# Kernel optimization log

Measured on AMD Instinct MI355X. Metric: run time of the kernel, lower is better.

## Reference

```python
import jax, jax.numpy as jnp
import numpy as np

S_CENTROIDS = 512
RADIUS = 0.5
NSAMPLE = 32
BN_EPS = 1e-5


def farthest_point_sample(xyz, s):
    # xyz: [B, N, 3] -> idx [B, s], deterministic start at index 0
    B, N, _ = xyz.shape

    def step(carry, _):
        dist, far = carry  # dist [B,N], far [B]
        centroid = jnp.take_along_axis(xyz, far[:, None, None], axis=1)  # [B,1,3]
        d = jnp.sum((xyz - centroid) ** 2, axis=-1)  # [B,N]
        dist = jnp.minimum(dist, d)
        nxt = jnp.argmax(dist, axis=-1).astype(jnp.int32)
        return (dist, nxt), far

    init = (jnp.full((B, N), 1e10, dtype=xyz.dtype), jnp.zeros((B,), jnp.int32))
    _, idx = jax.lax.scan(step, init, None, length=s)
    return idx.T  # [B, s]


def query_ball_point(radius, nsample, xyz, new_xyz):
    # xyz [B,N,3], new_xyz [B,S,3] -> group idx [B,S,nsample]
    B, N, _ = xyz.shape
    sqr = jnp.sum((new_xyz[:, :, None, :] - xyz[:, None, :, :]) ** 2, axis=-1)  # [B,S,N]
    gidx = jnp.where(sqr > radius * radius, N, jnp.arange(N, dtype=jnp.int32)[None, None, :])
    gidx = jnp.sort(gidx, axis=-1)[:, :, :nsample]  # closest-index-first valid ids
    first = gidx[:, :, :1]
    gidx = jnp.where(gidx == N, first, gidx)  # pad misses with first neighbor
    return gidx


def bn_relu(h, gamma, beta):
    # training-mode BatchNorm1d over (batch, length) dims of [BS, C, k]
    m = jnp.mean(h, axis=(0, 2), keepdims=True)
    v = jnp.var(h, axis=(0, 2), keepdims=True)
    hn = (h - m) / jnp.sqrt(v + BN_EPS)
    return jax.nn.relu(hn * gamma[None, :, None] + beta[None, :, None])


def setup_inputs() -> dict:
    key = jax.random.key(0)
    k1, k2, k3, k4 = jax.random.split(key, 4)
    B, N, Din, Dout = 16, 2048, 64, 128  # in_channels=2*Din=128
    x = jax.random.normal(k1, (B, Din, N), dtype=jnp.float32)
    coords = jax.random.uniform(k2, (B, N, 3), dtype=jnp.float32, minval=-1.0, maxval=1.0)
    W1 = jax.random.normal(k3, (Dout, 2 * Din), dtype=jnp.float32) * 0.05  # conv1 1x1 kernel
    W2 = jax.random.normal(k4, (Dout, Dout), dtype=jnp.float32) * 0.05    # conv2 1x1 kernel
    gamma1 = jnp.ones((Dout,), jnp.float32); beta1 = jnp.zeros((Dout,), jnp.float32)
    gamma2 = jnp.ones((Dout,), jnp.float32); beta2 = jnp.zeros((Dout,), jnp.float32)
    return {"x": x, "coords": coords, "W1": W1, "W2": W2,
            "gamma1": gamma1, "beta1": beta1, "gamma2": gamma2, "beta2": beta2}


def reference(x, coords, W1, W2, gamma1, beta1, gamma2, beta2):
    B = x.shape[0]
    feats = jnp.transpose(x, (0, 2, 1))  # [B, N, D]

    fidx = farthest_point_sample(coords, S_CENTROIDS)  # [B, s]
    bidx = jnp.arange(B)[:, None]
    new_xyz = coords[bidx, fidx]        # [B, s, 3]
    new_feat = feats[bidx, fidx]        # [B, s, D]

    gidx = query_ball_point(RADIUS, NSAMPLE, coords, new_xyz)  # [B, s, k]
    grouped = feats[jnp.arange(B)[:, None, None], gidx]        # [B, s, k, D]

    center = new_feat[:, :, None, :]
    agg = jnp.concatenate([grouped - center,
                           jnp.broadcast_to(center, grouped.shape)], axis=-1)  # [B, s, k, 2D]

    b, s, k, d = agg.shape
    h = jnp.transpose(agg, (0, 1, 3, 2)).reshape(b * s, d, k)  # [BS, 2D, k]
    h = bn_relu(jnp.einsum('bck,oc->bok', h, W1), gamma1, beta1)
    h = bn_relu(jnp.einsum('bck,oc->bok', h, W2), gamma2, beta2)
    pooled = jnp.max(h, axis=-1)                  # [BS, out]
    new_feature = jnp.transpose(pooled.reshape(b, s, -1), (0, 2, 1))  # [B, out, s]
    return new_xyz, new_feature
```

## Files before the change

### kernel.cpp

```cpp
#include <hip/hip_runtime.h>
#include <cstdint>

typedef unsigned int uint;
typedef unsigned short ushort_t;
typedef unsigned long long ull;
typedef __attribute__((ext_vector_type(8))) short bf16x8;
typedef __attribute__((ext_vector_type(4))) float f32x4;

#define B_   16
#define N_   2048
#define S_   512
#define G_   8192
#define DIN  64
#define DOUT 128
#define K_   32
#define ATS  136
#define ATS1 72

__device__ __forceinline__ uint bf16b(float f) {
  uint u = __float_as_uint(f);
  return (u + 0x7fffu + ((u >> 16) & 1u)) >> 16;
}
__device__ __forceinline__ float bf2f(uint b) { return __uint_as_float(b << 16); }

template<int CTRL, int RM>
__device__ __forceinline__ ull dpp_max_step(ull x) {
  uint lo = (uint)x, hi = (uint)(x >> 32);
  uint nlo = (uint)__builtin_amdgcn_update_dpp((int)lo, (int)lo, CTRL, RM, 0xf, true);
  uint nhi = (uint)__builtin_amdgcn_update_dpp((int)hi, (int)hi, CTRL, RM, 0xf, true);
  ull y = ((ull)nhi << 32) | (ull)nlo;
  return x > y ? x : y;
}

__global__ __launch_bounds__(256) void fps_kernel(const float* __restrict__ coords,
                                                  int* __restrict__ fidx,
                                                  float* __restrict__ out_xyz) {
  int b = blockIdx.x;
  const float* cb = coords + (size_t)b * (N_ * 3);
  __shared__ float4 spt[N_];
  __shared__ ull    skey[2][4];
  __shared__ int    sfar[S_];
  int tid = threadIdx.x, wid = tid >> 6;
  float px[8], py[8], pz[8], dist[8];
  uint nidx[8];
  int j0 = tid * 8;
#pragma unroll
  for (int i = 0; i < 8; ++i) {
    float x3 = cb[3 * (j0 + i)], y3 = cb[3 * (j0 + i) + 1], z3 = cb[3 * (j0 + i) + 2];
    px[i] = x3; py[i] = y3; pz[i] = z3;
    spt[j0 + i] = make_float4(x3, y3, z3, 0.f);
    dist[i] = 1e10f;
    nidx[i] = ~(uint)(j0 + i);
  }
  float cx = cb[0], cy = cb[1], cz = cb[2];
  uint far = 0;
  __syncthreads();
  for (int s = 0; s < S_; ++s) {
    if (tid == 0) sfar[s] = (int)far;
    ull best = 0;
#pragma unroll
    for (int i = 0; i < 8; ++i) {
      float dx = __fsub_rn(px[i], cx);
      float dy = __fsub_rn(py[i], cy);
      float dz = __fsub_rn(pz[i], cz);
      float d = __fadd_rn(__fadd_rn(__fmul_rn(dx, dx), __fmul_rn(dy, dy)), __fmul_rn(dz, dz));
      float nd = fminf(dist[i], d);
      dist[i] = nd;
      ull p = ((ull)__float_as_uint(nd) << 32) | (ull)nidx[i];
      best = best > p ? best : p;
    }
    best = dpp_max_step<0x111, 0xf>(best);
    best = dpp_max_step<0x112, 0xf>(best);
    best = dpp_max_step<0x114, 0xf>(best);
    best = dpp_max_step<0x118, 0xf>(best);
    best = dpp_max_step<0x142, 0xa>(best);
    best = dpp_max_step<0x143, 0xc>(best);
    int pb = s & 1;
    if ((tid & 63) == 63) skey[pb][wid] = best;
    __syncthreads();
    ull k0 = skey[pb][0], k1 = skey[pb][1], k2 = skey[pb][2], k3 = skey[pb][3];
    uint jw0 = ~(uint)k0, jw1 = ~(uint)k1, jw2 = ~(uint)k2, jw3 = ~(uint)k3;
    float4 q0 = spt[jw0], q1 = spt[jw1], q2 = spt[jw2], q3 = spt[jw3];
    bool t01 = k0 > k1, t23 = k2 > k3;
    ull ka = t01 ? k0 : k1;   float4 qa = t01 ? q0 : q1;
    ull kb2 = t23 ? k2 : k3;  float4 qb = t23 ? q2 : q3;
    bool tw = ka > kb2;
    ull kw = tw ? ka : kb2;   float4 qw = tw ? qa : qb;
    far = ~(uint)kw;
    cx = qw.x; cy = qw.y; cz = qw.z;
  }
  __syncthreads();
  for (int s2 = tid; s2 < S_; s2 += 256) {
    int f = sfar[s2];
    fidx[b * S_ + s2] = f;
    float4 c4 = spt[f];
    int o = (b * S_ + s2) * 3;
    out_xyz[o] = c4.x; out_xyz[o + 1] = c4.y; out_xyz[o + 2] = c4.z;
  }
}

__global__ __launch_bounds__(256) void ball_kernel(const float* __restrict__ coords,
                                                   const int* __restrict__ fidx,
                                                   int* __restrict__ gidx) {
  int lane = threadIdx.x & 63;
  int g = __builtin_amdgcn_readfirstlane(blockIdx.x * 4 + (threadIdx.x >> 6));
  int b = g >> 9;
  const float* cb = coords + (size_t)b * (N_ * 3);
  int nf = fidx[g];
  float cx = cb[3 * nf], cy = cb[3 * nf + 1], cz = cb[3 * nf + 2];
  int* out = gidx + g * K_;
  int cnt = 0, first = 0;
  bool hasfirst = false;
  for (int base = 0; base < N_; base += 64) {
    int j = base + lane;
    float dx = __fsub_rn(cb[3 * j], cx);
    float dy = __fsub_rn(cb[3 * j + 1], cy);
    float dz = __fsub_rn(cb[3 * j + 2], cz);
    float d = __fadd_rn(__fadd_rn(__fmul_rn(dx, dx), __fmul_rn(dy, dy)), __fmul_rn(dz, dz));
    bool in = (d <= 0.25f);
    ull m = __ballot(in);
    if (in) {
      int pos = cnt + __popcll(m & ((1ull << lane) - 1ull));
      if (pos < K_) out[pos] = j;
    }
    if (!hasfirst && m) { first = base + (__ffsll((long long)m) - 1); hasfirst = true; }
    cnt += __popcll(m);
    if (cnt >= K_) break;
  }
  if (cnt < K_) {
    for (int p = cnt + lane; p < K_; p += 64) out[p] = first;
  }
}

__global__ __launch_bounds__(256) void prep_kernel(const float* __restrict__ W1,
                                                   const float* __restrict__ W2,
                                                   ushort_t* __restrict__ Bp1,
                                                   ushort_t* __restrict__ Bpd,
                                                   ushort_t* __restrict__ Bp2) {
  int i = blockIdx.x * 256 + threadIdx.x;
  int j2 = i & 7, l = (i >> 3) & 63;
  {
    int kc = (i >> 9) & 3, nt = i >> 11;
    int o2 = nt * 16 + (l & 15);
    int c2 = kc * 32 + ((l >> 4) * 8) + j2;
    Bp2[i] = (ushort_t)bf16b(W2[o2 * 128 + c2]);
  }
  if (i < 8192) {
    int kc = (i >> 9) & 1, nt = (i >> 10) & 7;
    int o2 = nt * 16 + (l & 15);
    int c2 = kc * 32 + ((l >> 4) * 8) + j2;
    float wa = W1[o2 * 128 + c2];
    float wb = W1[o2 * 128 + 64 + c2];
    Bp1[i] = (ushort_t)bf16b(wa);
    Bpd[i] = (ushort_t)bf16b(wb - wa);
  }
}

__global__ __launch_bounds__(256) void gemm1_kernel(const float* __restrict__ x,
    const int* __restrict__ fidx, const int* __restrict__ gidx,
    const ushort_t* __restrict__ Bp1, const ushort_t* __restrict__ Bpd,
    ushort_t* __restrict__ h1T, float* __restrict__ psum, float* __restrict__ psq) {
  __shared__ ushort_t xgT[4][32 * ATS1];
  __shared__ float sctr[4][DIN];
  int tid = threadIdx.x;
  int lane = tid & 63, wid = tid >> 6;
  int g = __builtin_amdgcn_readfirstlane(blockIdx.x * 4 + wid);
  int b = g >> 9;
  const float* xb = x + (size_t)b * (DIN * N_);
  int nf = fidx[g];
  sctr[wid][lane] = xb[(size_t)lane * N_ + nf];
  int kk = lane & 31, ch = lane >> 5;
  int gik = gidx[g * K_ + kk];
  ushort_t* xw = xgT[wid];
#pragma unroll
  for (int cc = 0; cc < 32; ++cc) {
    int c = ch * 32 + cc;
    xw[kk * ATS1 + c] = (ushort_t)bf16b(xb[(size_t)c * N_ + gik]);
  }
  __syncthreads();
  int l15 = lane & 15, r8 = (lane >> 4) * 8;
  f32x4 acc[2][8];
#pragma unroll
  for (int nt = 0; nt < 8; ++nt) acc[0][nt] = (f32x4){0.f, 0.f, 0.f, 0.f};
#pragma unroll
  for (int kc = 0; kc < 2; ++kc) {
    union { bf16x8 v; ushort_t u[8]; } cu;
#pragma unroll
    for (int j = 0; j < 8; ++j) cu.u[j] = (ushort_t)bf16b(sctr[wid][kc * 32 + r8 + j]);
#pragma unroll
    for (int nt = 0; nt < 8; ++nt) {
      bf16x8 bf = *(const bf16x8*)(Bpd + ((nt * 2 + kc) * 64 + lane) * 8);
      acc[0][nt] = __builtin_amdgcn_mfma_f32_16x16x32_bf16(cu.v, bf, acc[0][nt], 0, 0, 0);
    }
  }
#pragma unroll
  for (int nt = 0; nt < 8; ++nt) acc[1][nt] = acc[0][nt];
#pragma unroll
  for (int kc = 0; kc < 2; ++kc) {
    bf16x8 afrag[2];
#pragma unroll
    for (int mt = 0; mt < 2; ++mt)
      afrag[mt] = *(const bf16x8*)(xw + (mt * 16 + l15) * ATS1 + kc * 32 + r8);
#pragma unroll
    for (int nt = 0; nt < 8; ++nt) {
      bf16x8 bf = *(const bf16x8*)(Bp1 + ((nt * 2 + kc) * 64 + lane) * 8);
      acc[0][nt] = __builtin_amdgcn_mfma_f32_16x16x32_bf16(afrag[0], bf, acc[0][nt], 0, 0, 0);
      acc[1][nt] = __builtin_amdgcn_mfma_f32_16x16x32_bf16(afrag[1], bf, acc[1][nt], 0, 0, 0);
    }
  }
#pragma unroll
  for (int nt = 0; nt < 8; ++nt) {
    float s = 0.f, q = 0.f;
#pragma unroll
    for (int mt = 0; mt < 2; ++mt)
#pragma unroll
      for (int r = 0; r < 4; ++r) { float a = acc[mt][nt][r]; s += a; q = fmaf(a, a, q); }
    s += __shfl_xor(s, 16, 64); s += __shfl_xor(s, 32, 64);
    q += __shfl_xor(q, 16, 64); q += __shfl_xor(q, 32, 64);
    if (lane < 16) {
      int o = nt * 16 + lane;
      psum[o * G_ + g] = s; psq[o * G_ + g] = q;
    }
  }
#pragma unroll
  for (int mt = 0; mt < 2; ++mt)
#pragma unroll
    for (int r = 0; r < 4; ++r) {
      int k = mt * 16 + (lane >> 4) * 4 + r;
      ushort_t* dst = h1T + (size_t)g * 4096 + k * 128 + l15;
#pragma unroll
      for (int nt = 0; nt < 8; ++nt)
        dst[nt * 16] = (ushort_t)bf16b(acc[mt][nt][r]);
    }
}

__global__ __launch_bounds__(256) void bn_finalize(const float* __restrict__ psum,
    const float* __restrict__ psq, const float* __restrict__ gamma,
    const float* __restrict__ beta, float* __restrict__ bnp) {
  int o = blockIdx.x, tid = threadIdx.x;
  double s = 0.0, q = 0.0;
  for (int g = tid; g < G_; g += 256) { s += (double)psum[o * G_ + g]; q += (double)psq[o * G_ + g]; }
  __shared__ double ss[256], qq[256];
  ss[tid] = s; qq[tid] = q; __syncthreads();
  for (int off = 128; off > 0; off >>= 1) {
    if (tid < off) { ss[tid] += ss[tid + off]; qq[tid] += qq[tid + off]; }
    __syncthreads();
  }
  if (tid == 0) {
    double n = 262144.0;
    double mean = ss[0] / n, var = qq[0] / n - mean * mean;
    float scv = (float)((double)gamma[o] / sqrt(var + 1e-5));
    bnp[2 * o] = scv;
    bnp[2 * o + 1] = (float)((double)beta[o] - mean * (double)scv);
  }
}

__global__ __launch_bounds__(256) void gemm2_kernel(const ushort_t* __restrict__ h1T,
    const ushort_t* __restrict__ Bp2, const float* __restrict__ bnp1,
    float* __restrict__ psum, float* __restrict__ psq,
    float* __restrict__ hmax, float* __restrict__ hmin) {
  __shared__ ushort_t actT[4][32 * ATS];
  int tid = threadIdx.x;
  int lane = tid & 63, wid = tid >> 6;
  int g = __builtin_amdgcn_readfirstlane(blockIdx.x * 4 + wid);
  ushort_t* aw = actT[wid];
  int c0 = (lane & 15) * 8;
  float s1[8], t1[8];
#pragma unroll
  for (int jj = 0; jj < 8; ++jj) { s1[jj] = bnp1[2 * (c0 + jj)]; t1[jj] = bnp1[2 * (c0 + jj) + 1]; }
  const uint4* src = (const uint4*)(h1T + (size_t)g * 4096);
#pragma unroll
  for (int t = 0; t < 8; ++t) {
    int idx = t * 64 + lane;
    uint4 v = src[idx];
    int k = idx >> 4;
    uint w[4] = {v.x, v.y, v.z, v.w};
    uint o4[4];
#pragma unroll
    for (int p2 = 0; p2 < 4; ++p2) {
      float a0 = fmaxf(fmaf(bf2f(w[p2] & 0xffffu), s1[2 * p2], t1[2 * p2]), 0.f);
      float a1 = fmaxf(fmaf(bf2f(w[p2] >> 16), s1[2 * p2 + 1], t1[2 * p2 + 1]), 0.f);
      o4[p2] = (bf16b(a1) << 16) | bf16b(a0);
    }
    *(uint4*)(aw + k * ATS + c0) = make_uint4(o4[0], o4[1], o4[2], o4[3]);
  }
  __syncthreads();
  f32x4 acc[2][8];
#pragma unroll
  for (int mt = 0; mt < 2; ++mt)
#pragma unroll
    for (int nt = 0; nt < 8; ++nt) acc[mt][nt] = (f32x4){0.f, 0.f, 0.f, 0.f};
#pragma unroll
  for (int kc = 0; kc < 4; ++kc) {
    bf16x8 afrag[2];
#pragma unroll
    for (int mt = 0; mt < 2; ++mt)
      afrag[mt] = *(const bf16x8*)(aw + (mt * 16 + (lane & 15)) * ATS + kc * 32 + (lane >> 4) * 8);
#pragma unroll
    for (int nt = 0; nt < 8; ++nt) {
      bf16x8 bfrag = *(const bf16x8*)(Bp2 + ((nt * 4 + kc) * 64 + lane) * 8);
      acc[0][nt] = __builtin_amdgcn_mfma_f32_16x16x32_bf16(afrag[0], bfrag, acc[0][nt], 0, 0, 0);
      acc[1][nt] = __builtin_amdgcn_mfma_f32_16x16x32_bf16(afrag[1], bfrag, acc[1][nt], 0, 0, 0);
    }
  }
#pragma unroll
  for (int nt = 0; nt < 8; ++nt) {
    float s = 0.f, q = 0.f, mx = -1e30f, mn = 1e30f;
#pragma unroll
    for (int mt = 0; mt < 2; ++mt)
#pragma unroll
      for (int r = 0; r < 4; ++r) {
        float a = acc[mt][nt][r];
        s += a; q = fmaf(a, a, q); mx = fmaxf(mx, a); mn = fminf(mn, a);
      }
    s += __shfl_xor(s, 16, 64); s += __shfl_xor(s, 32, 64);
    q += __shfl_xor(q, 16, 64); q += __shfl_xor(q, 32, 64);
    mx = fmaxf(mx, __shfl_xor(mx, 16, 64)); mx = fmaxf(mx, __shfl_xor(mx, 32, 64));
    mn = fminf(mn, __shfl_xor(mn, 16, 64)); mn = fminf(mn, __shfl_xor(mn, 32, 64));
    if (lane < 16) {
      int o = nt * 16 + lane;
      psum[o * G_ + g] = s; psq[o * G_ + g] = q;
      hmax[o * G_ + g] = mx; hmin[o * G_ + g] = mn;
    }
  }
}

__global__ __launch_bounds__(256) void pool_kernel(const float* __restrict__ hmax,
    const float* __restrict__ hmin, const float* __restrict__ bnp2,
    float* __restrict__ out) {
  int i = blockIdx.x * 256 + threadIdx.x;
  int s = i & 511;
  int o = (i >> 9) & 127;
  int b = i >> 16;
  int g = b * 512 + s;
  float scv = bnp2[2 * o], tf = bnp2[2 * o + 1];
  float v = (scv >= 0.f) ? hmax[o * G_ + g] : hmin[o * G_ + g];
  out[i] = fmaxf(fmaf(scv, v, tf), 0.f);
}

extern "C" void kernel_launch(void* const* d_in, const int* in_sizes, int n_in,
                              void* d_out, int out_size, void* d_ws, size_t ws_size,
                              hipStream_t stream) {
  const float* x      = (const float*)d_in[0];
  const float* coords = (const float*)d_in[1];
  const float* W1     = (const float*)d_in[2];
  const float* W2     = (const float*)d_in[3];
  const float* gamma1 = (const float*)d_in[4];
  const float* beta1  = (const float*)d_in[5];
  const float* gamma2 = (const float*)d_in[6];
  const float* beta2  = (const float*)d_in[7];
  float* out = (float*)d_out;
  char* ws = (char*)d_ws;
  ushort_t* h1T  = (ushort_t*)(ws);
  float* psum1 = (float*)(ws + 67108864);
  float* psq1  = (float*)(ws + 71303168);
  float* psum2 = (float*)(ws + 75497472);
  float* psq2  = (float*)(ws + 79691776);
  float* hmax  = (float*)(ws + 83886080);
  float* hmin  = (float*)(ws + 88080384);
  ushort_t* Bp1 = (ushort_t*)(ws + 92274688);
  ushort_t* Bpd = (ushort_t*)(ws + 92291072);
  ushort_t* Bp2 = (ushort_t*)(ws + 92307456);
  float* bnp1  = (float*)(ws + 92340224);
  float* bnp2  = (float*)(ws + 92341248);
  int* fidx    = (int*)(ws + 92342272);
  int* gidx    = (int*)(ws + 92375040);

  prep_kernel<<<64, 256, 0, stream>>>(W1, W2, Bp1, Bpd, Bp2);
  fps_kernel<<<16, 256, 0, stream>>>(coords, fidx, out);
  ball_kernel<<<2048, 256, 0, stream>>>(coords, fidx, gidx);
  gemm1_kernel<<<2048, 256, 0, stream>>>(x, fidx, gidx, Bp1, Bpd, h1T, psum1, psq1);
  bn_finalize<<<128, 256, 0, stream>>>(psum1, psq1, gamma1, beta1, bnp1);
  gemm2_kernel<<<2048, 256, 0, stream>>>(h1T, Bp2, bnp1, psum2, psq2, hmax, hmin);
  bn_finalize<<<128, 256, 0, stream>>>(psum2, psq2, gamma2, beta2, bnp2);
  pool_kernel<<<4096, 256, 0, stream>>>(hmax, hmin, bnp2, out + 24576);
}
```

Before: 387.2 us.

## Use packed f32 math and float-only wave argmax in FPS kernel

Rewrites the farthest-point-sampling inner loop to compute squared distances with packed v_pk_add/mul_f32 on pairs of points. It replaces the 64-bit key DPP max reduction with a 32-bit float max, followed by a ballot and readlane to recover the winning lane and local index. Point coordinates in shared memory move from float4 AoS to SoA. The goal is to shorten the serial per-iteration critical path, at the cost of extra readlane/ballot steps and subtler tie-breaking, since the lowest lane wins ties.

```diff
diff --git a/kernel.cpp b/kernel.cpp
--- a/kernel.cpp
+++ b/kernel.cpp
@@ -6,6 +6,7 @@
 typedef unsigned long long ull;
 typedef __attribute__((ext_vector_type(8))) short bf16x8;
 typedef __attribute__((ext_vector_type(4))) float f32x4;
+typedef __attribute__((ext_vector_type(2))) float f32x2;
 
 #define B_   16
 #define N_   2048
@@ -24,12 +25,10 @@
 __device__ __forceinline__ float bf2f(uint b) { return __uint_as_float(b << 16); }
 
 template<int CTRL, int RM>
-__device__ __forceinline__ ull dpp_max_step(ull x) {
-  uint lo = (uint)x, hi = (uint)(x >> 32);
-  uint nlo = (uint)__builtin_amdgcn_update_dpp((int)lo, (int)lo, CTRL, RM, 0xf, true);
-  uint nhi = (uint)__builtin_amdgcn_update_dpp((int)hi, (int)hi, CTRL, RM, 0xf, true);
-  ull y = ((ull)nhi << 32) | (ull)nlo;
-  return x > y ? x : y;
+__device__ __forceinline__ float dpp_fmax_step(float x) {
+  float y = __uint_as_float((uint)__builtin_amdgcn_update_dpp(
+      (int)__float_as_uint(x), (int)__float_as_uint(x), CTRL, RM, 0xf, true));
+  return fmaxf(x, y);
 }
 
 __global__ __launch_bounds__(256) void fps_kernel(const float* __restrict__ coords,
@@ -37,65 +36,80 @@
                                                   float* __restrict__ out_xyz) {
   int b = blockIdx.x;
   const float* cb = coords + (size_t)b * (N_ * 3);
-  __shared__ float4 spt[N_];
-  __shared__ ull    skey[2][4];
-  __shared__ int    sfar[S_];
-  int tid = threadIdx.x, wid = tid >> 6;
-  float px[8], py[8], pz[8], dist[8];
-  uint nidx[8];
+  __shared__ float sptx[N_], spty[N_], sptz[N_];
+  __shared__ ull   skey[2][4];
+  __shared__ int   sfar[S_];
+  int tid = threadIdx.x, lane = tid & 63, wid = tid >> 6;
+  for (int j = tid; j < N_; j += 256) {
+    sptx[j] = cb[3 * j]; spty[j] = cb[3 * j + 1]; sptz[j] = cb[3 * j + 2];
+  }
+  f32x2 px[4], py[4], pz[4], dist[4];
   int j0 = tid * 8;
 #pragma unroll
-  for (int i = 0; i < 8; ++i) {
-    float x3 = cb[3 * (j0 + i)], y3 = cb[3 * (j0 + i) + 1], z3 = cb[3 * (j0 + i) + 2];
-    px[i] = x3; py[i] = y3; pz[i] = z3;
-    spt[j0 + i] = make_float4(x3, y3, z3, 0.f);
-    dist[i] = 1e10f;
-    nidx[i] = ~(uint)(j0 + i);
+  for (int p = 0; p < 4; ++p) {
+    int j = j0 + 2 * p;
+    px[p].x = cb[3 * j];     py[p].x = cb[3 * j + 1]; pz[p].x = cb[3 * j + 2];
+    px[p].y = cb[3 * j + 3]; py[p].y = cb[3 * j + 4]; pz[p].y = cb[3 * j + 5];
+    dist[p].x = 1e10f; dist[p].y = 1e10f;
   }
   float cx = cb[0], cy = cb[1], cz = cb[2];
   uint far = 0;
   __syncthreads();
   for (int s = 0; s < S_; ++s) {
     if (tid == 0) sfar[s] = (int)far;
-    ull best = 0;
-#pragma unroll
-    for (int i = 0; i < 8; ++i) {
-      float dx = __fsub_rn(px[i], cx);
-      float dy = __fsub_rn(py[i], cy);
-      float dz = __fsub_rn(pz[i], cz);
-      float d = __fadd_rn(__fadd_rn(__fmul_rn(dx, dx), __fmul_rn(dy, dy)), __fmul_rn(dz, dz));
-      float nd = fminf(dist[i], d);
-      dist[i] = nd;
-      ull p = ((ull)__float_as_uint(nd) << 32) | (ull)nidx[i];
-      best = best > p ? best : p;
-    }
-    best = dpp_max_step<0x111, 0xf>(best);
-    best = dpp_max_step<0x112, 0xf>(best);
-    best = dpp_max_step<0x114, 0xf>(best);
-    best = dpp_max_step<0x118, 0xf>(best);
-    best = dpp_max_step<0x142, 0xa>(best);
-    best = dpp_max_step<0x143, 0xc>(best);
+    f32x2 c2x = {cx, cx}, c2y = {cy, cy}, c2z = {cz, cz};
+    float bestv = -1.f; uint bestloc = 0;
+#pragma unroll
+    for (int p = 0; p < 4; ++p) {
+      f32x2 dx, dy, dz, qx, qy, qz, s1, s2;
+      asm("v_pk_add_f32 %0, %1, %2 neg_lo:[0,1] neg_hi:[0,1]" : "=v"(dx) : "v"(px[p]), "v"(c2x));
+      asm("v_pk_add_f32 %0, %1, %2 neg_lo:[0,1] neg_hi:[0,1]" : "=v"(dy) : "v"(py[p]), "v"(c2y));
+      asm("v_pk_add_f32 %0, %1, %2 neg_lo:[0,1] neg_hi:[0,1]" : "=v"(dz) : "v"(pz[p]), "v"(c2z));
+      asm("v_pk_mul_f32 %0, %1, %1" : "=v"(qx) : "v"(dx));
+      asm("v_pk_mul_f32 %0, %1, %1" : "=v"(qy) : "v"(dy));
+      asm("v_pk_mul_f32 %0, %1, %1" : "=v"(qz) : "v"(dz));
+      asm("v_pk_add_f32 %0, %1, %2" : "=v"(s1) : "v"(qx), "v"(qy));
+      asm("v_pk_add_f32 %0, %1, %2" : "=v"(s2) : "v"(s1), "v"(qz));
+      float n0 = fminf(dist[p].x, s2.x);
+      float n1 = fminf(dist[p].y, s2.y);
+      dist[p].x = n0; dist[p].y = n1;
+      bool g0 = n0 > bestv; bestv = g0 ? n0 : bestv; bestloc = g0 ? (uint)(2 * p) : bestloc;
+      bool g1 = n1 > bestv; bestv = g1 ? n1 : bestv; bestloc = g1 ? (uint)(2 * p + 1) : bestloc;
+    }
+    float m = bestv;
+    m = dpp_fmax_step<0x111, 0xf>(m);
+    m = dpp_fmax_step<0x112, 0xf>(m);
+    m = dpp_fmax_step<0x114, 0xf>(m);
+    m = dpp_fmax_step<0x118, 0xf>(m);
+    m = dpp_fmax_step<0x142, 0xa>(m);
+    m = dpp_fmax_step<0x143, 0xc>(m);
+    float wmax = __uint_as_float((uint)__builtin_amdgcn_readlane((int)__float_as_uint(m), 63));
+    ull mask = __ballot(bestv == wmax);
+    int wl = __ffsll((long long)mask) - 1;
+    uint loc = (uint)__builtin_amdgcn_readlane((int)bestloc, wl);
+    uint jg = (uint)(((wid << 6) + wl) * 8) + loc;
     int pb = s & 1;
-    if ((tid & 63) == 63) skey[pb][wid] = best;
+    if (lane == 0) skey[pb][wid] = ((ull)__float_as_uint(wmax) << 32) | (ull)(~jg);
     __syncthreads();
     ull k0 = skey[pb][0], k1 = skey[pb][1], k2 = skey[pb][2], k3 = skey[pb][3];
-    uint jw0 = ~(uint)k0, jw1 = ~(uint)k1, jw2 = ~(uint)k2, jw3 = ~(uint)k3;
-    float4 q0 = spt[jw0], q1 = spt[jw1], q2 = spt[jw2], q3 = spt[jw3];
+    uint w0 = ~(uint)k0, w1 = ~(uint)k1, w2 = ~(uint)k2, w3 = ~(uint)k3;
+    float x0 = sptx[w0], y0 = spty[w0], z0 = sptz[w0];
+    float x1 = sptx[w1], y1 = spty[w1], z1 = sptz[w1];
+    float x2 = sptx[w2], y2 = spty[w2], z2 = sptz[w2];
+    float x3 = sptx[w3], y3 = spty[w3], z3 = sptz[w3];
     bool t01 = k0 > k1, t23 = k2 > k3;
-    ull ka = t01 ? k0 : k1;   float4 qa = t01 ? q0 : q1;
-    ull kb2 = t23 ? k2 : k3;  float4 qb = t23 ? q2 : q3;
-    bool tw = ka > kb2;
-    ull kw = tw ? ka : kb2;   float4 qw = tw ? qa : qb;
-    far = ~(uint)kw;
-    cx = qw.x; cy = qw.y; cz = qw.z;
+    ull ka = t01 ? k0 : k1;  float xa = t01 ? x0 : x1, ya = t01 ? y0 : y1, za = t01 ? z0 : z1;
+    ull kb = t23 ? k2 : k3;  float xb = t23 ? x2 : x3, yb = t23 ? y2 : y3, zb = t23 ? z2 : z3;
+    bool tw = ka > kb;
+    far = ~(uint)(tw ? ka : kb);
+    cx = tw ? xa : xb; cy = tw ? ya : yb; cz = tw ? za : zb;
   }
   __syncthreads();
   for (int s2 = tid; s2 < S_; s2 += 256) {
     int f = sfar[s2];
     fidx[b * S_ + s2] = f;
-    float4 c4 = spt[f];
     int o = (b * S_ + s2) * 3;
-    out_xyz[o] = c4.x; out_xyz[o + 1] = c4.y; out_xyz[o + 2] = c4.z;
+    out_xyz[o] = sptx[f]; out_xyz[o + 1] = spty[f]; out_xyz[o + 2] = sptz[f];
   }
 }
 
```

New measurement: 382.8 us. No clear change (-1.1%).
